# Optimization experiments

Hardware: AMD Instinct MI355X
Metric: run time of the kernel (lower is better)

Reference implementation:

```python
import jax, jax.numpy as jnp
import numpy as np

N_ACC = 100000   # accounts
N_TX = 300000    # transactions
E = 600000       # edges per edge type
H = 256          # hidden_dim
TX_IN = 32
ACC_IN = 16
L = 2            # conv_layers
M = 300000       # edges to classify
BN_EPS = 1e-5


def setup_inputs() -> dict:
    key = jax.random.key(0)
    ks = jax.random.split(key, 24)
    def nrm(k, shape, scale=1.0):
        return jax.random.normal(k, shape, jnp.float32) * scale
    inp = {}
    inp["x_acc"] = nrm(ks[0], (N_ACC, ACC_IN))
    inp["x_tx"] = nrm(ks[1], (N_TX, TX_IN))
    inp["tx_raw"] = nrm(ks[2], (M, TX_IN))
    # edge type account -> transaction (row0: src account, row1: dst transaction)
    inp["ei_sends"] = jnp.stack([jax.random.randint(ks[3], (E,), 0, N_ACC),
                                 jax.random.randint(ks[4], (E,), 0, N_TX)])
    # edge type transaction -> account
    inp["ei_recv"] = jnp.stack([jax.random.randint(ks[5], (E,), 0, N_TX),
                                jax.random.randint(ks[6], (E,), 0, N_ACC)])
    inp["sender_idx"] = jax.random.randint(ks[7], (M,), 0, N_ACC)
    inp["receiver_idx"] = jax.random.randint(ks[8], (M,), 0, N_ACC)
    # input projections (torch Linear: y = x @ W.T + b)
    inp["W_acc"] = nrm(ks[9], (H, ACC_IN), ACC_IN ** -0.5)
    inp["b_acc"] = jnp.zeros((H,), jnp.float32)
    inp["W_tx"] = nrm(ks[10], (H, TX_IN), TX_IN ** -0.5)
    inp["b_tx"] = jnp.zeros((H,), jnp.float32)
    s = H ** -0.5
    # SAGEConv params per layer: _at = acc->tx edge type, _ta = tx->acc edge type
    # Wl: applied to mean-aggregated neighbor messages (has bias), Wr: root/self weight (no bias)
    inp["Wl_at"] = nrm(ks[11], (L, H, H), s); inp["bl_at"] = jnp.zeros((L, H), jnp.float32)
    inp["Wr_at"] = nrm(ks[12], (L, H, H), s)
    inp["Wl_ta"] = nrm(ks[13], (L, H, H), s); inp["bl_ta"] = jnp.zeros((L, H), jnp.float32)
    inp["Wr_ta"] = nrm(ks[14], (L, H, H), s)
    # shared BatchNorm1d per layer (inference mode: running stats)
    inp["bn_gamma"] = jnp.ones((L, H), jnp.float32)
    inp["bn_beta"] = jnp.zeros((L, H), jnp.float32)
    inp["bn_mean"] = nrm(ks[15], (L, H), 0.1)
    inp["bn_var"] = jax.random.uniform(ks[16], (L, H), jnp.float32, 0.5, 1.5)
    # edge MLP: Linear(2H+TX_IN -> H), ReLU, Linear(H -> 1)
    inp["W1"] = nrm(ks[17], (H, 2 * H + TX_IN), (2 * H + TX_IN) ** -0.5)
    inp["b1"] = jnp.zeros((H,), jnp.float32)
    inp["W2"] = nrm(ks[18], (1, H), s)
    inp["b2"] = jnp.zeros((1,), jnp.float32)
    return inp


def _sage(x_src, x_dst, ei, Wl, bl, Wr):
    # PyG SAGEConv: lin_l(mean_{j in N(i)} x_src[j]) + lin_r(x_dst[i])
    src, dst = ei[0], ei[1]
    n_dst = x_dst.shape[0]
    msg = x_src[src]                                                   # [E, H] gather
    agg = jax.ops.segment_sum(msg, dst, num_segments=n_dst)           # [N_dst, H] scatter-add
    cnt = jax.ops.segment_sum(jnp.ones((ei.shape[1],), x_src.dtype), dst, num_segments=n_dst)
    mean = agg / jnp.maximum(cnt, 1.0)[:, None]
    return mean @ Wl.T + bl + x_dst @ Wr.T


def _bn(v, g, b, m, var):
    return (v - m) * (g * jax.lax.rsqrt(var + BN_EPS)) + b


def reference(x_acc, x_tx, tx_raw, ei_sends, ei_recv, sender_idx, receiver_idx,
              W_acc, b_acc, W_tx, b_tx,
              Wl_at, bl_at, Wr_at, Wl_ta, bl_ta, Wr_ta,
              bn_gamma, bn_beta, bn_mean, bn_var,
              W1, b1, W2, b2):
    acc = jax.nn.relu(x_acc @ W_acc.T + b_acc)
    tx = jax.nn.relu(x_tx @ W_tx.T + b_tx)
    for l in range(L):
        # HeteroConv(aggr='sum'): each node type receives from exactly one edge type here
        tx_new = _sage(acc, tx, ei_sends, Wl_at[l], bl_at[l], Wr_at[l])
        acc_new = _sage(tx, acc, ei_recv, Wl_ta[l], bl_ta[l], Wr_ta[l])
        acc = jax.nn.relu(_bn(acc_new, bn_gamma[l], bn_beta[l], bn_mean[l], bn_var[l]))
        tx = jax.nn.relu(_bn(tx_new, bn_gamma[l], bn_beta[l], bn_mean[l], bn_var[l]))
    h_sender = acc[sender_idx]      # [M, H]
    h_receiver = acc[receiver_idx]  # [M, H]
    edge_repr = jnp.concatenate([h_sender, h_receiver, tx_raw], axis=1)  # [M, 2H+TX_IN]
    h = jax.nn.relu(edge_repr @ W1.T + b1)
    return (h @ W2.T + b2)[:, 0]    # [M]
```

## Files before the change

kernel.cpp:

```cpp
#include <hip/hip_runtime.h>
#include <hip/hip_bf16.h>

#define H 256
#define NACC 100000
#define NTX  300000
#define NE   600000
#define NM   300000

typedef unsigned short u16;
typedef unsigned int u32;
typedef __bf16 bf16x8 __attribute__((ext_vector_type(8)));
typedef float f32x4 __attribute__((ext_vector_type(4)));

__device__ __forceinline__ float bf2f(u32 u) {
    union { u32 i; float f; } v; v.i = u << 16; return v.f;
}
__device__ __forceinline__ u16 f2bf(float f) {
    union { float f; u32 i; } v; v.f = f;
    u32 r = v.i + 0x7FFFu + ((v.i >> 16) & 1u);
    return (u16)(r >> 16);
}
__device__ __forceinline__ u32 pk2(float a, float b) {
    return (u32)f2bf(a) | ((u32)f2bf(b) << 16);
}
__device__ __forceinline__ void acc8(float* s, uint4 v) {
    s[0] += bf2f(v.x & 0xffff); s[1] += bf2f(v.x >> 16);
    s[2] += bf2f(v.y & 0xffff); s[3] += bf2f(v.y >> 16);
    s[4] += bf2f(v.z & 0xffff); s[5] += bf2f(v.z >> 16);
    s[6] += bf2f(v.w & 0xffff); s[7] += bf2f(v.w >> 16);
}

__global__ void fillz_kernel(u32* __restrict__ p, long long n) {
    long long i = (long long)blockIdx.x * blockDim.x + threadIdx.x;
    long long st = (long long)gridDim.x * blockDim.x;
    for (; i < n; i += st) p[i] = 0u;
}

__global__ void wcat_kernel(const float* __restrict__ Wl, const float* __restrict__ Wr,
                            u16* __restrict__ dst) {
    int c = blockIdx.x, t = threadIdx.x;
    dst[(size_t)c * 512 + t]       = f2bf(Wl[(size_t)c * 256 + t]);
    dst[(size_t)c * 512 + 256 + t] = f2bf(Wr[(size_t)c * 256 + t]);
}
__global__ void wcat_frag_kernel(const float* __restrict__ Wl, const float* __restrict__ Wr,
                                 u16* __restrict__ dst) {
    int c = blockIdx.x, k = threadIdx.x;
    float v = (k < 256) ? Wl[(size_t)c * 256 + k] : Wr[(size_t)c * 256 + (k - 256)];
    int kstep = k >> 5, kg = (k & 31) >> 3, j = k & 7;
    dst[(size_t)((kstep * 16 + (c >> 4)) * 64 + kg * 16 + (c & 15)) * 8 + j] = f2bf(v);
}
__global__ void w1frag_kernel(const float* __restrict__ W1, u16* __restrict__ dst) {
    int c = blockIdx.x;
    for (int k = threadIdx.x; k < 544; k += 256) {
        float v = W1[(size_t)c * 544 + k];
        int kstep = k >> 5, kg = (k & 31) >> 3, j = k & 7;
        dst[(size_t)((kstep * 16 + (c >> 4)) * 64 + kg * 16 + (c & 15)) * 8 + j] = f2bf(v);
    }
}
__global__ void wproj_kernel(const float* __restrict__ W, u16* __restrict__ dst, int K) {
    int c = blockIdx.x, t = threadIdx.x;
    dst[(size_t)c * 32 + t] = (t < K) ? f2bf(W[(size_t)c * K + t]) : (u16)0;
}
__global__ void bnprep_kernel(const float* __restrict__ bl, const float* __restrict__ g,
                              const float* __restrict__ be, const float* __restrict__ m,
                              const float* __restrict__ v,
                              float* __restrict__ S, float* __restrict__ B) {
    int c = threadIdx.x;
    float s = g[c] * rsqrtf(v[c] + 1e-5f);
    S[c] = s;
    B[c] = (bl[c] - m[c]) * s + be[c];
}

template <int KK>
__launch_bounds__(256)
__global__ void proj_mfma(const float* __restrict__ x, const u16* __restrict__ Wb,
                          const float* __restrict__ b, u16* __restrict__ out, int N) {
    __shared__ __align__(16) u16 Af[8][64][8];
    __shared__ __align__(16) u16 Bf[16][64][8];
    int tid = threadIdx.x;
    int w = tid >> 6, lane = tid & 63;
    int row0 = blockIdx.x * 128;
    {
        int r = tid >> 1, h = tid & 1;
        int gr = row0 + r;
        int rt = r >> 4, rr = r & 15;
        uint4 p0 = make_uint4(0, 0, 0, 0), p1 = p0;
        if (gr < N && (KK == 32 || h == 0)) {
            const float* xp = x + (size_t)gr * KK + h * 16;
            float4 f0 = *(const float4*)(xp);
            float4 f1 = *(const float4*)(xp + 4);
            float4 f2 = *(const float4*)(xp + 8);
            float4 f3 = *(const float4*)(xp + 12);
            p0 = make_uint4(pk2(f0.x, f0.y), pk2(f0.z, f0.w), pk2(f1.x, f1.y), pk2(f1.z, f1.w));
            p1 = make_uint4(pk2(f2.x, f2.y), pk2(f2.z, f2.w), pk2(f3.x, f3.y), pk2(f3.z, f3.w));
        }
        int kg0 = 2 * h;
        *(uint4*)(&Af[rt][(kg0 * 16 + rr) ^ (kg0 << 2)][0]) = p0;
        *(uint4*)(&Af[rt][((kg0 + 1) * 16 + rr) ^ ((kg0 + 1) << 2)][0]) = p1;
    }
    {
        const u16* wp = Wb + (size_t)tid * 32;
#pragma unroll
        for (int q = 0; q < 4; ++q) {
            uint4 wv = *(const uint4*)(wp + q * 8);
            *(uint4*)(&Bf[tid >> 4][q * 16 + (tid & 15)][0]) = wv;
        }
    }
    __syncthreads();
    int arslot = lane ^ ((lane >> 4) << 2);
    f32x4 acc[8][4];
#pragma unroll
    for (int rt = 0; rt < 8; ++rt) {
        bf16x8 afr = *(const bf16x8*)(&Af[rt][arslot][0]);
#pragma unroll
        for (int ct = 0; ct < 4; ++ct) {
            bf16x8 bfr = *(const bf16x8*)(&Bf[w * 4 + ct][lane][0]);
            acc[rt][ct] = __builtin_amdgcn_mfma_f32_16x16x32_bf16(
                afr, bfr, (f32x4){0.f, 0.f, 0.f, 0.f}, 0, 0, 0);
        }
    }
    int rb = (lane >> 4) * 4, cc = lane & 15;
#pragma unroll
    for (int ct = 0; ct < 4; ++ct) {
        int cg = (w * 4 + ct) * 16 + cc;
        float bv = b[cg];
#pragma unroll
        for (int rt = 0; rt < 8; ++rt)
#pragma unroll
            for (int q = 0; q < 4; ++q) {
                int r = row0 + rt * 16 + rb + q;
                if (r < N)
                    out[(size_t)r * H + cg] = f2bf(fmaxf(acc[rt][ct][q] + bv, 0.0f));
            }
    }
}

__global__ void count_kernel(const int* __restrict__ dst, int E, int* __restrict__ cnt) {
    int e = blockIdx.x * blockDim.x + threadIdx.x;
    if (e < E) atomicAdd(&cnt[dst[e]], 1);
}
__global__ void scan1_kernel(const int* __restrict__ cnt, int N,
                             int* __restrict__ loc, int* __restrict__ bsum) {
    __shared__ int sh[256];
    int b = blockIdx.x, t = threadIdx.x;
    int base = b * 1024 + t * 4;
    int v0 = (base + 0 < N) ? cnt[base + 0] : 0;
    int v1 = (base + 1 < N) ? cnt[base + 1] : 0;
    int v2 = (base + 2 < N) ? cnt[base + 2] : 0;
    int v3 = (base + 3 < N) ? cnt[base + 3] : 0;
    int s = v0 + v1 + v2 + v3;
    sh[t] = s;
    __syncthreads();
    for (int o = 1; o < 256; o <<= 1) {
        int y = (t >= o) ? sh[t - o] : 0;
        __syncthreads();
        sh[t] += y;
        __syncthreads();
    }
    int run = sh[t] - s;
    if (base + 0 < N) loc[base + 0] = run; run += v0;
    if (base + 1 < N) loc[base + 1] = run; run += v1;
    if (base + 2 < N) loc[base + 2] = run; run += v2;
    if (base + 3 < N) loc[base + 3] = run;
    if (t == 0) bsum[b] = sh[255];
}
__global__ void scan2_kernel(int* __restrict__ bsum, int nb) {
    __shared__ int sh[1024];
    int t = threadIdx.x;
    int v = (t < nb) ? bsum[t] : 0;
    sh[t] = v;
    __syncthreads();
    for (int o = 1; o < 1024; o <<= 1) {
        int y = (t >= o) ? sh[t - o] : 0;
        __syncthreads();
        sh[t] += y;
        __syncthreads();
    }
    if (t < nb) bsum[t] = sh[t] - v;
}
__global__ void scan3_kernel(int* __restrict__ ptr, const int* __restrict__ bsum,
                             int N, int total) {
    int i = blockIdx.x * blockDim.x + threadIdx.x;
    if (i < N) ptr[i] += bsum[i >> 10];
    else if (i == N) ptr[N] = total;
}
__global__ void fillcsr_kernel(const int* __restrict__ src, const int* __restrict__ dst, int E,
                               const int* __restrict__ ptr, int* __restrict__ cur,
                               int* __restrict__ perm) {
    int e = blockIdx.x * blockDim.x + threadIdx.x;
    if (e < E) {
        int d = dst[e];
        int pos = ptr[d] + atomicAdd(&cur[d], 1);
        perm[pos] = src[e];
    }
}

template <int WS>
__launch_bounds__(256)
__global__ void gmean_kernel(const u16* __restrict__ feat, int fstride,
                             const int* __restrict__ ptr, const int* __restrict__ perm,
                             u16* __restrict__ out, int ostride, int c0,
                             int rows, int lo) {
    constexpr int LPD = WS / 4;
    constexpr int DPB = 256 / LPD;
    int g = threadIdx.x / LPD;
    int ln = threadIdx.x % LPD;
    int w = blockIdx.x * DPB + g;
    if (w >= rows) return;
    int d = lo + w;
    int e0 = ptr[d], e1 = ptr[d + 1];
    float a0 = 0.f, a1 = 0.f, a2 = 0.f, a3 = 0.f;
    for (int e = e0; e < e1; ++e) {
        int s = perm[e];
        uint2 v = *(const uint2*)(feat + (size_t)s * fstride + (ln << 2));
        a0 += bf2f(v.x & 0xffff); a1 += bf2f(v.x >> 16);
        a2 += bf2f(v.y & 0xffff); a3 += bf2f(v.y >> 16);
    }
    int deg = e1 - e0;
    float sc = (deg > 0) ? (1.0f / (float)deg) : 0.0f;
    uint2 pk;
    pk.x = pk2(a0 * sc, a1 * sc);
    pk.y = pk2(a2 * sc, a3 * sc);
    *(uint2*)(out + (size_t)w * ostride + c0 + (ln << 2)) = pk;
}

template <int K, int NC>
__launch_bounds__(256)
__global__ void proj2_kernel(const float* __restrict__ x, const float* __restrict__ W,
                             const float* __restrict__ b, u16* __restrict__ out,
                             int N, int c0, int ost) {
    __shared__ float xs[128][K + 4];
    constexpr int NG = 512 / NC;
    constexpr int RPT = 128 / NG;
    int tid = threadIdx.x;
    int row0 = blockIdx.x * 128;
    constexpr int NF4 = 128 * K / 4;
    for (int f = tid; f < NF4; f += 256) {
        int r = f / (K / 4), kq = (f % (K / 4)) * 4;
        int gr = row0 + r;
        float4 v = (gr < N) ? *(const float4*)(x + (size_t)gr * K + kq)
                            : make_float4(0.f, 0.f, 0.f, 0.f);
        *(float4*)&xs[r][kq] = v;
    }
    int lt2 = (tid % (NC / 2)) * 2;
    int g = tid / (NC / 2);
    float wa[K], wb[K];
    const float* wpa = W + (size_t)(c0 + lt2) * K;
#pragma unroll
    for (int k = 0; k < K; k += 4) {
        float4 va = *(const float4*)(wpa + k);
        float4 vb = *(const float4*)(wpa + K + k);
        wa[k] = va.x; wa[k + 1] = va.y; wa[k + 2] = va.z; wa[k + 3] = va.w;
        wb[k] = vb.x; wb[k + 1] = vb.y; wb[k + 2] = vb.z; wb[k + 3] = vb.w;
    }
    float b0 = b[c0 + lt2], b1 = b[c0 + lt2 + 1];
    __syncthreads();
#pragma unroll
    for (int rr = 0; rr < RPT; ++rr) {
        int r = g * RPT + rr;
        int gr = row0 + r;
        float a0 = b0, a1 = b1;
#pragma unroll
        for (int k = 0; k < K; k += 4) {
            float4 xv = *(const float4*)&xs[r][k];
            a0 += xv.x * wa[k] + xv.y * wa[k + 1] + xv.z * wa[k + 2] + xv.w * wa[k + 3];
            a1 += xv.x * wb[k] + xv.y * wb[k + 1] + xv.z * wb[k + 2] + xv.w * wb[k + 3];
        }
        if (gr < N) {
            u32 pk = (u32)f2bf(fmaxf(a0, 0.f)) | ((u32)f2bf(fmaxf(a1, 0.f)) << 16);
            *(u32*)(out + (size_t)gr * ost + lt2) = pk;
        }
    }
}

__launch_bounds__(512)
__global__ void combine_gather(const u16* __restrict__ featG, const int* __restrict__ ptr,
                               const int* __restrict__ perm, const u16* __restrict__ xd,
                               const u16* __restrict__ WcF,
                               const float* __restrict__ bnS, const float* __restrict__ bnB,
                               u16* __restrict__ outF, int rows) {
    __shared__ __align__(16) u16 Am[8][4][64][8];
    int tid = threadIdx.x;
    int w = tid >> 6, lane = tid & 63;
    int row0 = blockIdx.x * 64;

    {
        int r = tid >> 3, g = tid & 7;
        int grow = row0 + r;
        float s[32];
#pragma unroll
        for (int i = 0; i < 32; ++i) s[i] = 0.0f;
        float inv = 0.0f;
        if (grow < rows) {
            int e0 = ptr[grow], e1 = ptr[grow + 1];
            int dg = e1 - e0;
            inv = (dg > 0) ? 1.0f / (float)dg : 0.0f;
            int e = e0;
            for (; e + 1 < e1; e += 2) {
                int n0 = perm[e], n1 = perm[e + 1];
                const u16* p0 = featG + (size_t)n0 * H + g * 32;
                const u16* p1 = featG + (size_t)n1 * H + g * 32;
#pragma unroll
                for (int q = 0; q < 4; ++q) {
                    uint4 v0 = *(const uint4*)(p0 + q * 8);
                    uint4 v1 = *(const uint4*)(p1 + q * 8);
                    acc8(s + q * 8, v0);
                    acc8(s + q * 8, v1);
                }
            }
            if (e < e1) {
                int n0 = perm[e];
                const u16* p0 = featG + (size_t)n0 * H + g * 32;
#pragma unroll
                for (int q = 0; q < 4; ++q)
                    acc8(s + q * 8, *(const uint4*)(p0 + q * 8));
            }
        }
        int rt = r >> 4, rr = r & 15;
#pragma unroll
        for (int q = 0; q < 4; ++q) {
            int kgg = g * 4 + q;
            int kbs = kgg >> 2, akg = kgg & 3;
            uint4 pv;
            pv.x = pk2(s[q * 8 + 0] * inv, s[q * 8 + 1] * inv);
            pv.y = pk2(s[q * 8 + 2] * inv, s[q * 8 + 3] * inv);
            pv.z = pk2(s[q * 8 + 4] * inv, s[q * 8 + 5] * inv);
            pv.w = pk2(s[q * 8 + 6] * inv, s[q * 8 + 7] * inv);
            *(uint4*)(&Am[kbs][rt][(akg * 16 + rr) ^ (akg << 2)][0]) = pv;
        }
    }
    __syncthreads();

    int arslot = lane ^ ((lane >> 4) << 2);
    const u16* xrow[4];
#pragma unroll
    for (int rt = 0; rt < 4; ++rt) {
        int r = row0 + rt * 16 + (lane & 15);
        if (r > rows - 1) r = rows - 1;
        xrow[rt] = xd + (size_t)r * H + (lane >> 4) * 8;
    }
    const u16* wb = WcF + (size_t)lane * 8;

    f32x4 acc[4][2];
#pragma unroll
    for (int i = 0; i < 4; ++i) {
        acc[i][0] = (f32x4){0.f, 0.f, 0.f, 0.f};
        acc[i][1] = (f32x4){0.f, 0.f, 0.f, 0.f};
    }
#pragma unroll
    for (int ks = 0; ks < 8; ++ks) {
        bf16x8 afr[4];
#pragma unroll
        for (int rt = 0; rt < 4; ++rt)
            afr[rt] = *(const bf16x8*)(&Am[ks][rt][arslot][0]);
#pragma unroll
        for (int j = 0; j < 2; ++j) {
            bf16x8 bfr = *(const bf16x8*)(wb + (size_t)(ks * 16 + w * 2 + j) * 512);
#pragma unroll
            for (int rt = 0; rt < 4; ++rt)
                acc[rt][j] = __builtin_amdgcn_mfma_f32_16x16x32_bf16(afr[rt], bfr, acc[rt][j], 0, 0, 0);
        }
    }
#pragma unroll
    for (int ks = 8; ks < 16; ++ks) {
        bf16x8 afr[4];
#pragma unroll
        for (int rt = 0; rt < 4; ++rt)
            afr[rt] = *(const bf16x8*)(xrow[rt] + (ks - 8) * 32);
#pragma unroll
        for (int j = 0; j < 2; ++j) {
            bf16x8 bfr = *(const bf16x8*)(wb + (size_t)(ks * 16 + w * 2 + j) * 512);
#pragma unroll
            for (int rt = 0; rt < 4; ++rt)
                acc[rt][j] = __builtin_amdgcn_mfma_f32_16x16x32_bf16(afr[rt], bfr, acc[rt][j], 0, 0, 0);
        }
    }
    __syncthreads();
    int rb = (lane >> 4) * 4, cc = lane & 15;
#pragma unroll
    for (int j = 0; j < 2; ++j) {
        int cg = (w * 2 + j) * 16 + cc;
        float s = bnS[cg], sh = bnB[cg];
#pragma unroll
        for (int rt = 0; rt < 4; ++rt)
#pragma unroll
            for (int q = 0; q < 4; ++q) {
                int r = row0 + rt * 16 + rb + q;
                if (r < rows)
                    outF[(size_t)r * H + cg] = f2bf(fmaxf(acc[rt][j][q] * s + sh, 0.0f));
            }
    }
}

template <int COLS>
__launch_bounds__(256)
__global__ void combine_mfma(const u16* __restrict__ mean_, const u16* __restrict__ xd,
                             const u16* __restrict__ Wcat,
                             const float* __restrict__ bnS, const float* __restrict__ bnB,
                             u16* __restrict__ outF, int ostride, int out_c0,
                             int rows, int c0) {
    constexpr int NCT = COLS / 16;
    constexpr int CTW = NCT / 4;
    constexpr int PPT = (COLS * 4) / 256;
    __shared__ __align__(16) u16 Af[4][64][8];
    __shared__ __align__(16) u16 Bf[NCT][64][8];
    int tid = threadIdx.x;
    int w = tid >> 6, lane = tid & 63;
    int row0 = blockIdx.x * 64;
    int arow = tid >> 2, akg = tid & 3;
    bool arok = (row0 + arow) < rows;
    const u16* am = mean_ + (size_t)(row0 + arow) * H;
    const u16* ax = xd + (size_t)(row0 + arow) * H;
    int awslot = (akg * 16 + (arow & 15)) ^ (akg << 2);
    int arslot = lane ^ ((lane >> 4) << 2);
    int bc = tid % COLS;
    int bkg0 = (tid / COLS) * PPT;
    const u16* wp0 = Wcat + (size_t)(c0 + bc) * 512 + bkg0 * 8;

    f32x4 acc[4][CTW];
#pragma unroll
    for (int i = 0; i < 4; ++i)
#pragma unroll
        for (int j = 0; j < CTW; ++j) acc[i][j] = (f32x4){0.f, 0.f, 0.f, 0.f};

    for (int kb = 0; kb < 512; kb += 32) {
        uint4 av = make_uint4(0, 0, 0, 0);
        if (arok) {
            int kg = kb + akg * 8;
            av = (kg < 256) ? *(const uint4*)(am + kg) : *(const uint4*)(ax + (kg - 256));
        }
        *(uint4*)(&Af[arow >> 4][awslot][0]) = av;
#pragma unroll
        for (int q = 0; q < PPT; ++q) {
            uint4 wv = *(const uint4*)(wp0 + kb + q * 8);
            *(uint4*)(&Bf[bc >> 4][(bkg0 + q) * 16 + (bc & 15)][0]) = wv;
        }
        __syncthreads();
        bf16x8 afr[4];
#pragma unroll
        for (int rt = 0; rt < 4; ++rt)
            afr[rt] = *(const bf16x8*)(&Af[rt][arslot][0]);
#pragma unroll
        for (int ctl = 0; ctl < CTW; ++ctl) {
            bf16x8 b = *(const bf16x8*)(&Bf[w * CTW + ctl][lane][0]);
#pragma unroll
            for (int rt = 0; rt < 4; ++rt)
                acc[rt][ctl] = __builtin_amdgcn_mfma_f32_16x16x32_bf16(afr[rt], b, acc[rt][ctl], 0, 0, 0);
        }
        __syncthreads();
    }
    int rb = (lane >> 4) * 4;
    int ccol = lane & 15;
#pragma unroll
    for (int ctl = 0; ctl < CTW; ++ctl) {
        int clocal = (w * CTW + ctl) * 16 + ccol;
        int cg = c0 + clocal;
        float s = bnS[cg], sh = bnB[cg];
#pragma unroll
        for (int rt = 0; rt < 4; ++rt) {
#pragma unroll
            for (int q = 0; q < 4; ++q) {
                int r = row0 + rt * 16 + rb + q;
                if (r < rows)
                    outF[(size_t)r * ostride + out_c0 + clocal] = f2bf(fmaxf(acc[rt][ctl][q] * s + sh, 0.0f));
            }
        }
    }
}

__launch_bounds__(512)
__global__ void mlp_mfma(const u16* __restrict__ accF, const int* __restrict__ sidx,
                         const int* __restrict__ ridx, const float* __restrict__ txr,
                         const u16* __restrict__ W1F, const float* __restrict__ b1,
                         const float* __restrict__ W2, const float* __restrict__ b2,
                         float* __restrict__ out, int M) {
    __shared__ __align__(16) u16 Af[4][64][8];
    __shared__ float red[8][64];
    int tid = threadIdx.x;
    int w = tid >> 6, lane = tid & 63;
    int row0 = blockIdx.x * 64;
    int sr = tid >> 3, sg = tid & 7;
    int grow = row0 + sr;
    int gcl = (grow > M - 1) ? (M - 1) : grow;
    const u16* srow_s = accF + (size_t)sidx[gcl] * H + sg * 4;
    const u16* srow_r = accF + (size_t)ridx[gcl] * H + sg * 4;
    const float* tp = txr + (size_t)gcl * 32 + sg * 4;
    int rt_s = sr >> 4, rr_s = sr & 15;
    int akg = sg >> 1, hh = (sg & 1) * 4;
    u16* wslot = &Af[rt_s][(akg * 16 + rr_s) ^ (akg << 2)][hh];

    auto stage_load = [&](int ks) -> uint2 {
        if (ks < 8)  return *(const uint2*)(srow_s + ks * 32);
        if (ks < 16) return *(const uint2*)(srow_r + (ks - 8) * 32);
        float4 f = *(const float4*)tp;
        uint2 r;
        r.x = pk2(f.x, f.y); r.y = pk2(f.z, f.w);
        return r;
    };

    int arslot = lane ^ ((lane >> 4) << 2);
    const u16* wbs = W1F + (size_t)lane * 8;

    f32x4 acc[4][2];
#pragma unroll
    for (int i = 0; i < 4; ++i) {
        acc[i][0] = (f32x4){0.f, 0.f, 0.f, 0.f};
        acc[i][1] = (f32x4){0.f, 0.f, 0.f, 0.f};
    }

    uint2 reg = stage_load(0);
#pragma unroll
    for (int ks = 0; ks < 17; ++ks) {
        __syncthreads();
        *(uint2*)wslot = reg;
        __syncthreads();
        if (ks < 16) reg = stage_load(ks + 1);
        bf16x8 afr[4];
#pragma unroll
        for (int rt = 0; rt < 4; ++rt)
            afr[rt] = *(const bf16x8*)(&Af[rt][arslot][0]);
#pragma unroll
        for (int j = 0; j < 2; ++j) {
            bf16x8 bfr = *(const bf16x8*)(wbs + (size_t)(ks * 16 + w * 2 + j) * 512);
#pragma unroll
            for (int rt = 0; rt < 4; ++rt)
                acc[rt][j] = __builtin_amdgcn_mfma_f32_16x16x32_bf16(afr[rt], bfr, acc[rt][j], 0, 0, 0);
        }
    }
    float part[4][4];
#pragma unroll
    for (int rt = 0; rt < 4; ++rt)
#pragma unroll
        for (int q = 0; q < 4; ++q) part[rt][q] = 0.0f;
#pragma unroll
    for (int j = 0; j < 2; ++j) {
        int cg = (w * 2 + j) * 16 + (lane & 15);
        float b1v = b1[cg], w2v = W2[cg];
#pragma unroll
        for (int rt = 0; rt < 4; ++rt)
#pragma unroll
            for (int q = 0; q < 4; ++q)
                part[rt][q] += fmaxf(acc[rt][j][q] + b1v, 0.0f) * w2v;
    }
    int rb = (lane >> 4) * 4;
#pragma unroll
    for (int rt = 0; rt < 4; ++rt)
#pragma unroll
        for (int q = 0; q < 4; ++q) {
            float p = part[rt][q];
            p += __shfl_xor(p, 1);
            p += __shfl_xor(p, 2);
            p += __shfl_xor(p, 4);
            p += __shfl_xor(p, 8);
            if ((lane & 15) == 0) red[w][rt * 16 + rb + q] = p;
        }
    __syncthreads();
    if (tid < 64) {
        int r = row0 + tid;
        if (r < M)
            out[r] = red[0][tid] + red[1][tid] + red[2][tid] + red[3][tid]
                   + red[4][tid] + red[5][tid] + red[6][tid] + red[7][tid] + b2[0];
    }
}

static inline void fz(void* p, size_t bytes, hipStream_t s) {
    long long n = (long long)(bytes >> 2);
    int g = (int)(((n + 255) / 256 < 2048) ? (n + 255) / 256 : 2048);
    fillz_kernel<<<g, 256, 0, s>>>((u32*)p, n);
}
static inline size_t al256(size_t x) { return (x + 255) & ~(size_t)255; }

extern "C" void kernel_launch(void* const* d_in, const int* in_sizes, int n_in,
                              void* d_out, int out_size, void* d_ws, size_t ws_size,
                              hipStream_t stream) {
    const float* x_acc  = (const float*)d_in[0];
    const float* x_tx   = (const float*)d_in[1];
    const float* tx_raw = (const float*)d_in[2];
    const int* ei_sends = (const int*)d_in[3];
    const int* ei_recv  = (const int*)d_in[4];
    const int* sidx     = (const int*)d_in[5];
    const int* ridx     = (const int*)d_in[6];
    const float* W_acc  = (const float*)d_in[7];
    const float* b_acc  = (const float*)d_in[8];
    const float* W_tx   = (const float*)d_in[9];
    const float* b_tx   = (const float*)d_in[10];
    const float* Wl_at  = (const float*)d_in[11];
    const float* bl_at  = (const float*)d_in[12];
    const float* Wr_at  = (const float*)d_in[13];
    const float* Wl_ta  = (const float*)d_in[14];
    const float* bl_ta  = (const float*)d_in[15];
    const float* Wr_ta  = (const float*)d_in[16];
    const float* bng    = (const float*)d_in[17];
    const float* bnb    = (const float*)d_in[18];
    const float* bnm    = (const float*)d_in[19];
    const float* bnv    = (const float*)d_in[20];
    const float* W1     = (const float*)d_in[21];
    const float* b1     = (const float*)d_in[22];
    const float* W2     = (const float*)d_in[23];
    const float* b2     = (const float*)d_in[24];
    float* out = (float*)d_out;

    const size_t szFeatA = (size_t)NACC * H * 2;
    const size_t szFeatT = (size_t)NTX * H * 2;
    const size_t szCSR = al256((NTX + 1) * 4) + al256(4096) + al256((NTX + 1) * 4)
                       + al256((size_t)NE * 4) + al256((NACC + 1) * 4) + al256((size_t)NE * 4);
    const size_t szW = 3 * al256(256 * 512 * 2) + 3 * al256(16 * 16 * 64 * 8 * 2)
                     + al256(17 * 16 * 64 * 8 * 2)
                     + 2 * al256(3 * 256 * 4) + 2 * al256(256 * 32 * 2);

    size_t needF = szCSR + szW + 2 * al256(szFeatA) + al256(szFeatT) + 65536;
    auto needS = [&](int S, int CC) {
        return 3 * al256(szFeatA) + szCSR + szW + 2 * al256((size_t)CC * H * 2)
             + al256((size_t)NTX * (H / S) * 2) + 65536;
    };
    int plan, S = 2, CC = 16384;
    if (needF <= ws_size)                { plan = 0; }
    else if (needS(2, 16384) <= ws_size) { plan = 1; S = 2; CC = 16384; }
    else if (needS(4, 16384) <= ws_size) { plan = 1; S = 4; CC = 16384; }
    else                                 { plan = 1; S = 4; CC = 2048; }

    char* wsp = (char*)d_ws;
    size_t off = 0;
    auto alloc = [&](size_t bytes) -> void* {
        void* p = wsp + off;
        off = al256(off + bytes);
        return p;
    };
    int* cnt   = (int*)alloc((NTX + 1) * 4);
    int* bsum  = (int*)alloc(4096);
    int* ptrT  = (int*)alloc((NTX + 1) * 4);
    int* permS = (int*)alloc((size_t)NE * 4);
    int* ptrA  = (int*)alloc((NACC + 1) * 4);
    int* permR = (int*)alloc((size_t)NE * 4);
    u16* Wc[3];
    Wc[0] = (u16*)alloc(256 * 512 * 2);
    Wc[1] = (u16*)alloc(256 * 512 * 2);
    Wc[2] = (u16*)alloc(256 * 512 * 2);
    u16* WcF[3];
    WcF[0] = (u16*)alloc(16 * 16 * 64 * 8 * 2);
    WcF[1] = (u16*)alloc(16 * 16 * 64 * 8 * 2);
    WcF[2] = (u16*)alloc(16 * 16 * 64 * 8 * 2);
    u16* W1F = (u16*)alloc(17 * 16 * 64 * 8 * 2);
    float* bnS = (float*)alloc(3 * 256 * 4);
    float* bnB = (float*)alloc(3 * 256 * 4);
    u16* WbA = (u16*)alloc(256 * 32 * 2);
    u16* WbT = (u16*)alloc(256 * 32 * 2);
    u16* A0f = (u16*)alloc(szFeatA);
    u16* A1f = (u16*)alloc(szFeatA);

    wcat_kernel<<<256, 256, 0, stream>>>(Wl_ta, Wr_ta, Wc[0]);
    wcat_kernel<<<256, 256, 0, stream>>>(Wl_at, Wr_at, Wc[1]);
    wcat_kernel<<<256, 256, 0, stream>>>(Wl_ta + H * H, Wr_ta + H * H, Wc[2]);
    wcat_frag_kernel<<<256, 512, 0, stream>>>(Wl_ta, Wr_ta, WcF[0]);
    wcat_frag_kernel<<<256, 512, 0, stream>>>(Wl_at, Wr_at, WcF[1]);
    wcat_frag_kernel<<<256, 512, 0, stream>>>(Wl_ta + H * H, Wr_ta + H * H, WcF[2]);
    w1frag_kernel<<<256, 256, 0, stream>>>(W1, W1F);
    wproj_kernel<<<256, 32, 0, stream>>>(W_acc, WbA, 16);
    wproj_kernel<<<256, 32, 0, stream>>>(W_tx, WbT, 32);
    bnprep_kernel<<<1, 256, 0, stream>>>(bl_ta, bng, bnb, bnm, bnv, bnS, bnB);
    bnprep_kernel<<<1, 256, 0, stream>>>(bl_at, bng, bnb, bnm, bnv, bnS + 256, bnB + 256);
    bnprep_kernel<<<1, 256, 0, stream>>>(bl_ta + H, bng + H, bnb + H, bnm + H, bnv + H,
                                         bnS + 512, bnB + 512);

    const int EG = (NE + 255) / 256;
    const int nbT = (NTX + 1023) / 1024, nbA = (NACC + 1023) / 1024;
    fz(cnt, (size_t)NTX * 4, stream);
    count_kernel<<<EG, 256, 0, stream>>>(ei_sends + NE, NE, cnt);
    scan1_kernel<<<nbT, 256, 0, stream>>>(cnt, NTX, ptrT, bsum);
    scan2_kernel<<<1, 1024, 0, stream>>>(bsum, nbT);
    scan3_kernel<<<(NTX + 256) / 256 + 1, 256, 0, stream>>>(ptrT, bsum, NTX, NE);
    fz(cnt, (size_t)NTX * 4, stream);
    fillcsr_kernel<<<EG, 256, 0, stream>>>(ei_sends, ei_sends + NE, NE, ptrT, cnt, permS);
    fz(cnt, (size_t)NACC * 4, stream);
    count_kernel<<<EG, 256, 0, stream>>>(ei_recv + NE, NE, cnt);
    scan1_kernel<<<nbA, 256, 0, stream>>>(cnt, NACC, ptrA, bsum);
    scan2_kernel<<<1, 1024, 0, stream>>>(bsum, nbA);
    scan3_kernel<<<(NACC + 256) / 256 + 1, 256, 0, stream>>>(ptrA, bsum, NACC, NE);
    fz(cnt, (size_t)NACC * 4, stream);
    fillcsr_kernel<<<EG, 256, 0, stream>>>(ei_recv, ei_recv + NE, NE, ptrA, cnt, permR);

    proj_mfma<16><<<(NACC + 127) / 128, 256, 0, stream>>>(x_acc, WbA, b_acc, A0f, NACC);

    const int gA = (NACC + 63) / 64, gM = (NM + 63) / 64;

    if (plan == 0) {
        u16* T = (u16*)alloc(szFeatT);
        proj_mfma<32><<<(NTX + 127) / 128, 256, 0, stream>>>(x_tx, WbT, b_tx, T, NTX);
        combine_gather<<<gA, 512, 0, stream>>>(T, ptrA, permR, A0f, WcF[0], bnS, bnB, A1f, NACC);
        combine_gather<<<(NTX + 63) / 64, 512, 0, stream>>>(A0f, ptrT, permS, T, WcF[1],
                                                            bnS + 256, bnB + 256, T, NTX);
        combine_gather<<<gA, 512, 0, stream>>>(T, ptrA, permR, A1f, WcF[2],
                                               bnS + 512, bnB + 512, A0f, NACC);
        mlp_mfma<<<gM, 512, 0, stream>>>(A0f, sidx, ridx, tx_raw, W1F, b1, W2, b2, out, NM);
    } else {
        u16* meanbuf = (u16*)alloc(szFeatA);
        u16* T0c     = (u16*)alloc((size_t)CC * H * 2);
        u16* meanTc  = (u16*)alloc((size_t)CC * H * 2);
        const int WSL = H / S;
        u16* Tslice  = (u16*)alloc((size_t)NTX * WSL * 2);

        for (int s = 0; s < S; ++s) {
            int c0 = s * WSL;
            if (WSL == 128)
                proj2_kernel<32, 128><<<(NTX + 127) / 128, 256, 0, stream>>>(x_tx, W_tx, b_tx, Tslice, NTX, c0, WSL);
            else
                proj2_kernel<32, 64><<<(NTX + 127) / 128, 256, 0, stream>>>(x_tx, W_tx, b_tx, Tslice, NTX, c0, WSL);
            if (WSL == 128)
                gmean_kernel<128><<<(NACC + 7) / 8, 256, 0, stream>>>(Tslice, WSL, ptrA, permR, meanbuf, H, c0, NACC, 0);
            else
                gmean_kernel<64><<<(NACC + 15) / 16, 256, 0, stream>>>(Tslice, WSL, ptrA, permR, meanbuf, H, c0, NACC, 0);
        }
        combine_mfma<256><<<gA, 256, 0, stream>>>(meanbuf, A0f, Wc[0], bnS, bnB, A1f, H, 0, NACC, 0);
        for (int s = 0; s < S; ++s) {
            int c0 = s * WSL;
            for (int lo = 0; lo < NTX; lo += CC) {
                int cur = (NTX - lo < CC) ? (NTX - lo) : CC;
                proj2_kernel<32, 256><<<(cur + 127) / 128, 256, 0, stream>>>(x_tx + (size_t)lo * 32, W_tx, b_tx, T0c, cur, 0, H);
                gmean_kernel<256><<<(cur + 3) / 4, 256, 0, stream>>>(A0f, H, ptrT, permS, meanTc, H, 0, cur, lo);
                if (WSL == 128)
                    combine_mfma<128><<<(cur + 63) / 64, 256, 0, stream>>>(
                        meanTc, T0c, Wc[1], bnS + 256, bnB + 256,
                        Tslice + (size_t)lo * WSL, WSL, 0, cur, c0);
                else
                    combine_mfma<64><<<(cur + 63) / 64, 256, 0, stream>>>(
                        meanTc, T0c, Wc[1], bnS + 256, bnB + 256,
                        Tslice + (size_t)lo * WSL, WSL, 0, cur, c0);
            }
            if (WSL == 128)
                gmean_kernel<128><<<(NACC + 7) / 8, 256, 0, stream>>>(Tslice, WSL, ptrA, permR, meanbuf, H, c0, NACC, 0);
            else
                gmean_kernel<64><<<(NACC + 15) / 16, 256, 0, stream>>>(Tslice, WSL, ptrA, permR, meanbuf, H, c0, NACC, 0);
        }
        combine_mfma<256><<<gA, 256, 0, stream>>>(meanbuf, A1f, Wc[2], bnS + 512, bnB + 512, A0f, H, 0, NACC, 0);
        mlp_mfma<<<gM, 512, 0, stream>>>(A0f, sidx, ridx, tx_raw, W1F, b1, W2, b2, out, NM);
    }
}
```

Baseline: 961.7 us.

## Batch setup kernels, deepen gather unroll for account aggregation, raise occupancy bounds

Merges the per-config weight-prep, BN-prep, count and CSR-fill launches into single multi-config kernels indexed by blockIdx.y, and gives the two edge types separate count buffers so both CSRs build without extra zero fills. The wcat launches now run only in the non-default plan. Account-side combine_gather gets a 4-way unrolled neighbor gather for more loads in flight, and combine_gather and mlp_mfma get a min-blocks hint of 8 in __launch_bounds__. The occupancy hint may force register spills, and the cuts in small launches save only a little fixed overhead.

```diff
diff --git a/kernel.cpp b/kernel.cpp
--- a/kernel.cpp
+++ b/kernel.cpp
@@ -42,8 +42,14 @@
     dst[(size_t)c * 512 + t]       = f2bf(Wl[(size_t)c * 256 + t]);
     dst[(size_t)c * 512 + 256 + t] = f2bf(Wr[(size_t)c * 256 + t]);
 }
-__global__ void wcat_frag_kernel(const float* __restrict__ Wl, const float* __restrict__ Wr,
-                                 u16* __restrict__ dst) {
+__global__ void wcat_frag3_kernel(const float* __restrict__ Wl0, const float* __restrict__ Wr0,
+                                  const float* __restrict__ Wl1, const float* __restrict__ Wr1,
+                                  const float* __restrict__ Wl2, const float* __restrict__ Wr2,
+                                  u16* __restrict__ d0, u16* __restrict__ d1, u16* __restrict__ d2) {
+    int cfg = blockIdx.y;
+    const float* Wl = (cfg == 0) ? Wl0 : (cfg == 1) ? Wl1 : Wl2;
+    const float* Wr = (cfg == 0) ? Wr0 : (cfg == 1) ? Wr1 : Wr2;
+    u16* dst = (cfg == 0) ? d0 : (cfg == 1) ? d1 : d2;
     int c = blockIdx.x, k = threadIdx.x;
     float v = (k < 256) ? Wl[(size_t)c * 256 + k] : Wr[(size_t)c * 256 + (k - 256)];
     int kstep = k >> 5, kg = (k & 31) >> 3, j = k & 7;
@@ -57,18 +63,22 @@
         dst[(size_t)((kstep * 16 + (c >> 4)) * 64 + kg * 16 + (c & 15)) * 8 + j] = f2bf(v);
     }
 }
-__global__ void wproj_kernel(const float* __restrict__ W, u16* __restrict__ dst, int K) {
+__global__ void wproj2_kernel(const float* __restrict__ Wa, const float* __restrict__ Wt,
+                              u16* __restrict__ dA, u16* __restrict__ dT) {
     int c = blockIdx.x, t = threadIdx.x;
-    dst[(size_t)c * 32 + t] = (t < K) ? f2bf(W[(size_t)c * K + t]) : (u16)0;
-}
-__global__ void bnprep_kernel(const float* __restrict__ bl, const float* __restrict__ g,
-                              const float* __restrict__ be, const float* __restrict__ m,
-                              const float* __restrict__ v,
-                              float* __restrict__ S, float* __restrict__ B) {
-    int c = threadIdx.x;
-    float s = g[c] * rsqrtf(v[c] + 1e-5f);
-    S[c] = s;
-    B[c] = (bl[c] - m[c]) * s + be[c];
+    if (blockIdx.y == 0) dA[(size_t)c * 32 + t] = (t < 16) ? f2bf(Wa[(size_t)c * 16 + t]) : (u16)0;
+    else                 dT[(size_t)c * 32 + t] = f2bf(Wt[(size_t)c * 32 + t]);
+}
+__global__ void bnprep3_kernel(const float* __restrict__ bl_ta, const float* __restrict__ bl_at,
+                               const float* __restrict__ g_, const float* __restrict__ be_,
+                               const float* __restrict__ m_, const float* __restrict__ v_,
+                               float* __restrict__ S, float* __restrict__ B) {
+    int cfg = blockIdx.x, c = threadIdx.x;
+    const float* bl = (cfg == 0) ? bl_ta : (cfg == 1) ? bl_at : (bl_ta + 256);
+    int po = (cfg == 2) ? 256 : 0;
+    float s = g_[po + c] * rsqrtf(v_[po + c] + 1e-5f);
+    S[cfg * 256 + c] = s;
+    B[cfg * 256 + c] = (bl[c] - m_[po + c]) * s + be_[po + c];
 }
 
 template <int KK>
@@ -135,9 +145,12 @@
     }
 }
 
-__global__ void count_kernel(const int* __restrict__ dst, int E, int* __restrict__ cnt) {
+__global__ void count2_kernel(const int* __restrict__ dstS, const int* __restrict__ dstR, int E,
+                              int* __restrict__ cntT, int* __restrict__ cntA) {
     int e = blockIdx.x * blockDim.x + threadIdx.x;
-    if (e < E) atomicAdd(&cnt[dst[e]], 1);
+    if (e >= E) return;
+    if (blockIdx.y == 0) atomicAdd(&cntT[dstS[e]], 1);
+    else                 atomicAdd(&cntA[dstR[e]], 1);
 }
 __global__ void scan1_kernel(const int* __restrict__ cnt, int N,
                              int* __restrict__ loc, int* __restrict__ bsum) {
@@ -184,14 +197,18 @@
     if (i < N) ptr[i] += bsum[i >> 10];
     else if (i == N) ptr[N] = total;
 }
-__global__ void fillcsr_kernel(const int* __restrict__ src, const int* __restrict__ dst, int E,
-                               const int* __restrict__ ptr, int* __restrict__ cur,
-                               int* __restrict__ perm) {
+__global__ void fillcsr2_kernel(const int* __restrict__ srcS, const int* __restrict__ dstS,
+                                const int* __restrict__ srcR, const int* __restrict__ dstR, int E,
+                                const int* __restrict__ ptrT, int* __restrict__ curT, int* __restrict__ permS,
+                                const int* __restrict__ ptrA, int* __restrict__ curA, int* __restrict__ permR) {
     int e = blockIdx.x * blockDim.x + threadIdx.x;
-    if (e < E) {
-        int d = dst[e];
-        int pos = ptr[d] + atomicAdd(&cur[d], 1);
-        perm[pos] = src[e];
+    if (e >= E) return;
+    if (blockIdx.y == 0) {
+        int d = dstS[e];
+        permS[ptrT[d] + atomicAdd(&curT[d], 1)] = srcS[e];
+    } else {
+        int d = dstR[e];
+        permR[ptrA[d] + atomicAdd(&curA[d], 1)] = srcR[e];
     }
 }
 
@@ -273,7 +290,8 @@
     }
 }
 
-__launch_bounds__(512)
+template <bool DEEP>
+__launch_bounds__(512, 8)
 __global__ void combine_gather(const u16* __restrict__ featG, const int* __restrict__ ptr,
                                const int* __restrict__ perm, const u16* __restrict__ xd,
                                const u16* __restrict__ WcF,
@@ -296,6 +314,26 @@
             int dg = e1 - e0;
             inv = (dg > 0) ? 1.0f / (float)dg : 0.0f;
             int e = e0;
+            if (DEEP) {
+                for (; e + 3 < e1; e += 4) {
+                    int n0 = perm[e], n1 = perm[e + 1], n2 = perm[e + 2], n3 = perm[e + 3];
+                    const u16* p0 = featG + (size_t)n0 * H + g * 32;
+                    const u16* p1 = featG + (size_t)n1 * H + g * 32;
+                    const u16* p2 = featG + (size_t)n2 * H + g * 32;
+                    const u16* p3 = featG + (size_t)n3 * H + g * 32;
+#pragma unroll
+                    for (int q = 0; q < 4; ++q) {
+                        uint4 v0 = *(const uint4*)(p0 + q * 8);
+                        uint4 v1 = *(const uint4*)(p1 + q * 8);
+                        uint4 v2 = *(const uint4*)(p2 + q * 8);
+                        uint4 v3 = *(const uint4*)(p3 + q * 8);
+                        acc8(s + q * 8, v0);
+                        acc8(s + q * 8, v1);
+                        acc8(s + q * 8, v2);
+                        acc8(s + q * 8, v3);
+                    }
+                }
+            }
             for (; e + 1 < e1; e += 2) {
                 int n0 = perm[e], n1 = perm[e + 1];
                 const u16* p0 = featG + (size_t)n0 * H + g * 32;
@@ -468,7 +506,7 @@
     }
 }
 
-__launch_bounds__(512)
+__launch_bounds__(512, 8)
 __global__ void mlp_mfma(const u16* __restrict__ accF, const int* __restrict__ sidx,
                          const int* __restrict__ ridx, const float* __restrict__ txr,
                          const u16* __restrict__ W1F, const float* __restrict__ b1,
@@ -602,8 +640,9 @@
 
     const size_t szFeatA = (size_t)NACC * H * 2;
     const size_t szFeatT = (size_t)NTX * H * 2;
-    const size_t szCSR = al256((NTX + 1) * 4) + al256(4096) + al256((NTX + 1) * 4)
-                       + al256((size_t)NE * 4) + al256((NACC + 1) * 4) + al256((size_t)NE * 4);
+    const size_t szCSR = al256((NTX + 1) * 4) + al256((NACC + 1) * 4) + al256(4096)
+                       + al256((NTX + 1) * 4) + al256((NACC + 1) * 4)
+                       + 2 * al256((size_t)NE * 4);
     const size_t szW = 3 * al256(256 * 512 * 2) + 3 * al256(16 * 16 * 64 * 8 * 2)
                      + al256(17 * 16 * 64 * 8 * 2)
                      + 2 * al256(3 * 256 * 4) + 2 * al256(256 * 32 * 2);
@@ -626,11 +665,12 @@
         off = al256(off + bytes);
         return p;
     };
-    int* cnt   = (int*)alloc((NTX + 1) * 4);
+    int* cntT  = (int*)alloc((NTX + 1) * 4);
+    int* cntA  = (int*)alloc((NACC + 1) * 4);
     int* bsum  = (int*)alloc(4096);
     int* ptrT  = (int*)alloc((NTX + 1) * 4);
+    int* ptrA  = (int*)alloc((NACC + 1) * 4);
     int* permS = (int*)alloc((size_t)NE * 4);
-    int* ptrA  = (int*)alloc((NACC + 1) * 4);
     int* permR = (int*)alloc((size_t)NE * 4);
     u16* Wc[3];
     Wc[0] = (u16*)alloc(256 * 512 * 2);
@@ -648,36 +688,28 @@
     u16* A0f = (u16*)alloc(szFeatA);
     u16* A1f = (u16*)alloc(szFeatA);
 
-    wcat_kernel<<<256, 256, 0, stream>>>(Wl_ta, Wr_ta, Wc[0]);
-    wcat_kernel<<<256, 256, 0, stream>>>(Wl_at, Wr_at, Wc[1]);
-    wcat_kernel<<<256, 256, 0, stream>>>(Wl_ta + H * H, Wr_ta + H * H, Wc[2]);
-    wcat_frag_kernel<<<256, 512, 0, stream>>>(Wl_ta, Wr_ta, WcF[0]);
-    wcat_frag_kernel<<<256, 512, 0, stream>>>(Wl_at, Wr_at, WcF[1]);
-    wcat_frag_kernel<<<256, 512, 0, stream>>>(Wl_ta + H * H, Wr_ta + H * H, WcF[2]);
+    const size_t cntBytes = al256((NTX + 1) * 4) + al256((NACC + 1) * 4);
+
+    wcat_frag3_kernel<<<dim3(256, 3), 512, 0, stream>>>(
+        Wl_ta, Wr_ta, Wl_at, Wr_at, Wl_ta + H * H, Wr_ta + H * H, WcF[0], WcF[1], WcF[2]);
     w1frag_kernel<<<256, 256, 0, stream>>>(W1, W1F);
-    wproj_kernel<<<256, 32, 0, stream>>>(W_acc, WbA, 16);
-    wproj_kernel<<<256, 32, 0, stream>>>(W_tx, WbT, 32);
-    bnprep_kernel<<<1, 256, 0, stream>>>(bl_ta, bng, bnb, bnm, bnv, bnS, bnB);
-    bnprep_kernel<<<1, 256, 0, stream>>>(bl_at, bng, bnb, bnm, bnv, bnS + 256, bnB + 256);
-    bnprep_kernel<<<1, 256, 0, stream>>>(bl_ta + H, bng + H, bnb + H, bnm + H, bnv + H,
-                                         bnS + 512, bnB + 512);
+    wproj2_kernel<<<dim3(256, 2), 32, 0, stream>>>(W_acc, W_tx, WbA, WbT);
+    bnprep3_kernel<<<3, 256, 0, stream>>>(bl_ta, bl_at, bng, bnb, bnm, bnv, bnS, bnB);
 
     const int EG = (NE + 255) / 256;
     const int nbT = (NTX + 1023) / 1024, nbA = (NACC + 1023) / 1024;
-    fz(cnt, (size_t)NTX * 4, stream);
-    count_kernel<<<EG, 256, 0, stream>>>(ei_sends + NE, NE, cnt);
-    scan1_kernel<<<nbT, 256, 0, stream>>>(cnt, NTX, ptrT, bsum);
+    fz(cntT, cntBytes, stream);
+    count2_kernel<<<dim3(EG, 2), 256, 0, stream>>>(ei_sends + NE, ei_recv + NE, NE, cntT, cntA);
+    scan1_kernel<<<nbT, 256, 0, stream>>>(cntT, NTX, ptrT, bsum);
     scan2_kernel<<<1, 1024, 0, stream>>>(bsum, nbT);
     scan3_kernel<<<(NTX + 256) / 256 + 1, 256, 0, stream>>>(ptrT, bsum, NTX, NE);
-    fz(cnt, (size_t)NTX * 4, stream);
-    fillcsr_kernel<<<EG, 256, 0, stream>>>(ei_sends, ei_sends + NE, NE, ptrT, cnt, permS);
-    fz(cnt, (size_t)NACC * 4, stream);
-    count_kernel<<<EG, 256, 0, stream>>>(ei_recv + NE, NE, cnt);
-    scan1_kernel<<<nbA, 256, 0, stream>>>(cnt, NACC, ptrA, bsum);
+    scan1_kernel<<<nbA, 256, 0, stream>>>(cntA, NACC, ptrA, bsum);
     scan2_kernel<<<1, 1024, 0, stream>>>(bsum, nbA);
     scan3_kernel<<<(NACC + 256) / 256 + 1, 256, 0, stream>>>(ptrA, bsum, NACC, NE);
-    fz(cnt, (size_t)NACC * 4, stream);
-    fillcsr_kernel<<<EG, 256, 0, stream>>>(ei_recv, ei_recv + NE, NE, ptrA, cnt, permR);
+    fz(cntT, cntBytes, stream);
+    fillcsr2_kernel<<<dim3(EG, 2), 256, 0, stream>>>(
+        ei_sends, ei_sends + NE, ei_recv, ei_recv + NE, NE,
+        ptrT, cntT, permS, ptrA, cntA, permR);
 
     proj_mfma<16><<<(NACC + 127) / 128, 256, 0, stream>>>(x_acc, WbA, b_acc, A0f, NACC);
 
@@ -686,13 +718,16 @@
     if (plan == 0) {
         u16* T = (u16*)alloc(szFeatT);
         proj_mfma<32><<<(NTX + 127) / 128, 256, 0, stream>>>(x_tx, WbT, b_tx, T, NTX);
-        combine_gather<<<gA, 512, 0, stream>>>(T, ptrA, permR, A0f, WcF[0], bnS, bnB, A1f, NACC);
-        combine_gather<<<(NTX + 63) / 64, 512, 0, stream>>>(A0f, ptrT, permS, T, WcF[1],
-                                                            bnS + 256, bnB + 256, T, NTX);
-        combine_gather<<<gA, 512, 0, stream>>>(T, ptrA, permR, A1f, WcF[2],
-                                               bnS + 512, bnB + 512, A0f, NACC);
+        combine_gather<true><<<gA, 512, 0, stream>>>(T, ptrA, permR, A0f, WcF[0], bnS, bnB, A1f, NACC);
+        combine_gather<false><<<(NTX + 63) / 64, 512, 0, stream>>>(A0f, ptrT, permS, T, WcF[1],
+                                                                   bnS + 256, bnB + 256, T, NTX);
+        combine_gather<true><<<gA, 512, 0, stream>>>(T, ptrA, permR, A1f, WcF[2],
+                                                     bnS + 512, bnB + 512, A0f, NACC);
         mlp_mfma<<<gM, 512, 0, stream>>>(A0f, sidx, ridx, tx_raw, W1F, b1, W2, b2, out, NM);
     } else {
+        wcat_kernel<<<256, 256, 0, stream>>>(Wl_ta, Wr_ta, Wc[0]);
+        wcat_kernel<<<256, 256, 0, stream>>>(Wl_at, Wr_at, Wc[1]);
+        wcat_kernel<<<256, 256, 0, stream>>>(Wl_ta + H * H, Wr_ta + H * H, Wc[2]);
         u16* meanbuf = (u16*)alloc(szFeatA);
         u16* T0c     = (u16*)alloc((size_t)CC * H * 2);
         u16* meanTc  = (u16*)alloc((size_t)CC * H * 2);
```

New measurement: 1.674 ms. 1.74x slower.
